# Kernel optimization log

Measured on AMD Instinct MI355X. Metric: run time of the kernel, lower is better.

## Reference

```python
import jax, jax.numpy as jnp
import numpy as np

N_NODES = 100000


def _gcn_conv(x, W, b, src, dst, deg_inv_sqrt):
    # linear transform first (PyG GCNConv order): [N, F] @ [F, H]
    h = x @ W
    # symmetric normalization per edge: deg^-1/2[src] * deg^-1/2[dst]
    norm = deg_inv_sqrt[src] * deg_inv_sqrt[dst]
    msg = h[src] * norm[:, None]  # [E, H]
    out = jax.ops.segment_sum(msg, dst, num_segments=N_NODES)
    return out + b


def setup_inputs() -> dict:
    key = jax.random.key(0)
    k1, k2, k3, k4 = jax.random.split(key, 4)
    F_IN, H = 512, 512
    E = 800000
    x = jax.random.normal(k1, (N_NODES, F_IN), dtype=jnp.float32)
    edge_index = jax.random.randint(k2, (2, E), 0, N_NODES, dtype=jnp.int64)
    W1 = jax.random.normal(k3, (F_IN, H), dtype=jnp.float32) * (1.0 / np.sqrt(F_IN))
    b1 = jnp.zeros((H,), dtype=jnp.float32)
    W2 = jax.random.normal(k4, (H, H), dtype=jnp.float32) * (1.0 / np.sqrt(H))
    b2 = jnp.zeros((H,), dtype=jnp.float32)
    return {"x": x, "edge_index": edge_index, "W1": W1, "b1": b1, "W2": W2, "b2": b2}


def reference(x, edge_index, W1, b1, W2, b2):
    # add self loops (PyG GCNConv default add_self_loops=True)
    loop = jnp.arange(N_NODES, dtype=edge_index.dtype)
    src = jnp.concatenate([edge_index[0], loop])
    dst = jnp.concatenate([edge_index[1], loop])
    # degree of destination nodes (including self loops)
    deg = jax.ops.segment_sum(jnp.ones_like(dst, dtype=x.dtype), dst, num_segments=N_NODES)
    deg_inv_sqrt = jnp.where(deg > 0, jax.lax.rsqrt(jnp.maximum(deg, 1.0)), 0.0)
    h = jax.nn.relu(_gcn_conv(x, W1, b1, src, dst, deg_inv_sqrt))
    # dropout is identity at inference (training=False)
    out = _gcn_conv(h, W2, b2, src, dst, deg_inv_sqrt)
    return out
```

## Files before the change

### kernel.cpp

```cpp
#include <hip/hip_runtime.h>

#define N_NODES 100000
#define E_EDGES 800000
#define E_TOT   900000
#define F 512

typedef __attribute__((ext_vector_type(8))) short short8;
typedef __attribute__((ext_vector_type(4))) float f32x4;
typedef unsigned int u32;

__device__ __forceinline__ float bfu(unsigned int u) {
    union { unsigned int i; float f; } c; c.i = u << 16; return c.f;
}
__device__ __forceinline__ unsigned short f2b(float f) {
    union { float f; unsigned int u; } c; c.f = f;
    return (unsigned short)((c.u + 0x7fffu + ((c.u >> 16) & 1u)) >> 16);
}
__device__ __forceinline__ float fbits(unsigned int u) {
    union { unsigned int i; float f; } c; c.i = u; return c.f;
}
__device__ __forceinline__ unsigned int bits(float f) {
    union { float f; unsigned int i; } c; c.f = f; return c.i;
}
__device__ __forceinline__ void gload_lds16(const void* g, void* l) {
    __builtin_amdgcn_global_load_lds(
        (const __attribute__((address_space(1))) u32*)g,
        (__attribute__((address_space(3))) u32*)l, 16, 0, 0);
}

__global__ void k_hist(const int* __restrict__ ei, unsigned int* deg) {
    int e = blockIdx.x * 256 + threadIdx.x;
    if (e < E_EDGES) atomicAdd(&deg[ei[E_EDGES + e]], 1u);
}

__global__ void k_disalloc(const unsigned int* __restrict__ deg, unsigned int* counter,
                           float* __restrict__ dis,
                           int2* __restrict__ seg, unsigned int* __restrict__ cursor) {
    int i = blockIdx.x * 256 + threadIdx.x;
    if (i < N_NODES) {
        unsigned int d = deg[i] + 1u;
        dis[i] = rsqrtf((float)d);
        unsigned int p = atomicAdd(counter, d);
        seg[i] = make_int2((int)p, (int)(p + d));
        cursor[i] = p;
    }
}

__global__ void k_scatter(const int* __restrict__ ei, const float* __restrict__ dis,
                          unsigned int* __restrict__ cursor,
                          uint2* __restrict__ ev) {
    int e = blockIdx.x * 256 + threadIdx.x;
    if (e < E_TOT) {
        int s, d;
        if (e < E_EDGES) { s = ei[e]; d = ei[E_EDGES + e]; }
        else             { s = e - E_EDGES; d = s; }
        unsigned int p = atomicAdd(&cursor[d], 1u);
        ev[p] = make_uint2((unsigned)s, bits(dis[s] * dis[d]));
    }
}

__global__ void k_cvtX(const float* __restrict__ xin, unsigned short* __restrict__ xb) {
    int i = blockIdx.x * 256 + threadIdx.x;
    const f32x4* p = (const f32x4*)xin + (size_t)i * 2;
    f32x4 a = __builtin_nontemporal_load(p);
    f32x4 b = __builtin_nontemporal_load(p + 1);
    uint4 o;
    o.x = (unsigned)f2b(a[0]) | ((unsigned)f2b(a[1]) << 16);
    o.y = (unsigned)f2b(a[2]) | ((unsigned)f2b(a[3]) << 16);
    o.z = (unsigned)f2b(b[0]) | ((unsigned)f2b(b[1]) << 16);
    o.w = (unsigned)f2b(b[2]) | ((unsigned)f2b(b[3]) << 16);
    *(uint4*)(xb + (size_t)i * 8) = o;
}

__global__ void k_cvtW(const float* __restrict__ W1, const float* __restrict__ W2,
                       unsigned short* __restrict__ W1t, unsigned short* __restrict__ W2t) {
    int t = blockIdx.x * 256 + threadIdx.x;
    int which = t >= F * F;
    int u = t - which * F * F;
    int n = u >> 9, k = u & 511;
    const float* W = which ? W2 : W1;
    unsigned short* Wt = which ? W2t : W1t;
    Wt[u] = f2b(W[k * F + n]);
}

__global__ __launch_bounds__(512, 4)
void gemm_bt(const unsigned short* __restrict__ A, const unsigned short* __restrict__ Bt,
             const float* __restrict__ bias,
             unsigned short* __restrict__ outb, float* __restrict__ outf,
             int relu, int M) {
    __shared__ unsigned short sm[24576];

    int nwg = gridDim.x * gridDim.y;
    int orig = blockIdx.y * gridDim.x + blockIdx.x;
    int q = nwg >> 3, r = nwg & 7;
    int xcd = orig & 7, j8 = orig >> 3;
    int wgid = (xcd < r ? xcd * (q + 1) : r * (q + 1) + (xcd - r) * q) + j8;
    int by = wgid & 3;
    int bx = wgid >> 2;

    int t  = threadIdx.x;
    int lane = t & 63, w = t >> 6;
    int wr = w >> 1, wc = w & 1;
    int rsel = lane & 15, khalf = (lane >> 4) * 8;

    f32x4 acc[4][4];
    #pragma unroll
    for (int m = 0; m < 4; ++m)
        #pragma unroll
        for (int n = 0; n < 4; ++n)
            acc[m][n] = (f32x4){0.f, 0.f, 0.f, 0.f};

    int rowBase = bx * 256;

    int arA[2], kcA[2];
    #pragma unroll
    for (int i = 0; i < 2; ++i) {
        int idx = i * 512 + t;
        int rr = idx >> 2;
        kcA[i] = (idx & 3) * 8;
        int ga = rowBase + rr; if (ga >= M) ga = M - 1;
        arA[i] = ga;
    }
    int brB = by * 128 + (t >> 2);
    int kcB = (t & 3) * 8;

    auto STAGE = [&](int buf, int k0) {
        gload_lds16(A + (size_t)arA[0] * F + k0 + kcA[0], sm + buf * 8192 + t * 8);
        gload_lds16(A + (size_t)arA[1] * F + k0 + kcA[1], sm + buf * 8192 + (512 + t) * 8);
        gload_lds16(Bt + (size_t)brB * F + k0 + kcB, sm + 16384 + buf * 4096 + t * 8);
    };
    auto COMPUTE = [&](int buf) {
        const unsigned short* la = sm + buf * 8192;
        const unsigned short* lb = sm + 16384 + buf * 4096;
        short8 bfr[4];
        #pragma unroll
        for (int n = 0; n < 4; ++n)
            bfr[n] = *(const short8*)&lb[(wc * 64 + n * 16 + rsel) * 32 + khalf];
        #pragma unroll
        for (int m = 0; m < 4; ++m) {
            short8 af = *(const short8*)&la[(wr * 64 + m * 16 + rsel) * 32 + khalf];
            #pragma unroll
            for (int n = 0; n < 4; ++n)
                acc[m][n] = __builtin_amdgcn_mfma_f32_16x16x32_bf16(af, bfr[n], acc[m][n], 0, 0, 0);
        }
    };

    STAGE(0, 0);
    __syncthreads();
    #pragma unroll
    for (int kp = 0; kp < 8; ++kp) {
        STAGE(1, (2 * kp + 1) * 32);
        COMPUTE(0);
        __syncthreads();
        if (kp < 7) STAGE(0, (2 * kp + 2) * 32);
        COMPUTE(1);
        __syncthreads();
    }

    int rq = (lane >> 4) * 4, cq = lane & 15;
    if (outb) {
        #pragma unroll
        for (int h = 0; h < 2; ++h) {
            if (h) __syncthreads();
            if ((wr >> 1) == h) {
                #pragma unroll
                for (int m = 0; m < 4; ++m)
                    #pragma unroll
                    for (int n = 0; n < 4; ++n) {
                        int cl = wc * 64 + n * 16 + cq;
                        float bv = bias[by * 128 + cl];
                        #pragma unroll
                        for (int j = 0; j < 4; ++j) {
                            int rl = (wr & 1) * 64 + m * 16 + rq + j;
                            float v = acc[m][n][j] + bv;
                            if (relu) v = fmaxf(v, 0.f);
                            sm[rl * 128 + cl] = f2b(v);
                        }
                    }
            }
            __syncthreads();
            #pragma unroll
            for (int p = 0; p < 4; ++p) {
                int sidx = (p * 512 + t) * 8;
                int row = sidx >> 7;
                int col = sidx & 127;
                int grow = rowBase + h * 128 + row;
                if (grow < M) {
                    uint4 v = *(const uint4*)&sm[sidx];
                    *(uint4*)&outb[(size_t)grow * F + by * 128 + col] = v;
                }
            }
        }
    } else {
        #pragma unroll
        for (int m = 0; m < 4; ++m)
            #pragma unroll
            for (int n = 0; n < 4; ++n) {
                int colv = by * 128 + wc * 64 + n * 16 + cq;
                float bv = bias[colv];
                #pragma unroll
                for (int j = 0; j < 4; ++j) {
                    int row = rowBase + wr * 64 + m * 16 + rq + j;
                    if (row < M) {
                        float v = acc[m][n][j] + bv;
                        if (relu) v = fmaxf(v, 0.f);
                        __builtin_nontemporal_store(v, outf + (size_t)row * F + colv);
                    }
                }
            }
    }
}

#define LOADP(k) uint2 p##k = ev[e + k]
#define LOADV(k) uint4 v##k = *(const uint4*)(base + ((size_t)p##k.x << 9))
#define ACCV(k)  { float w_ = fbits(p##k.y); \
    acc[0] += w_ * bfu(v##k.x & 0xffffu); acc[1] += w_ * bfu(v##k.x >> 16); \
    acc[2] += w_ * bfu(v##k.y & 0xffffu); acc[3] += w_ * bfu(v##k.y >> 16); \
    acc[4] += w_ * bfu(v##k.z & 0xffffu); acc[5] += w_ * bfu(v##k.z >> 16); \
    acc[6] += w_ * bfu(v##k.w & 0xffffu); acc[7] += w_ * bfu(v##k.w >> 16); }

__global__ __launch_bounds__(256)
void k_agg(const unsigned short* __restrict__ hin, const int2* __restrict__ seg,
           const uint2* __restrict__ ev,
           unsigned short* __restrict__ outb) {
    int node = blockIdx.x * 4 + (threadIdx.x >> 6);
    int lane = threadIdx.x & 63;
    if (node >= N_NODES) return;
    int2 se = seg[node];
    int e0 = se.x, e1 = se.y;
    float acc[8] = {0, 0, 0, 0, 0, 0, 0, 0};
    const unsigned short* base = hin + lane * 8;

    int e = e0;
    int n8 = e0 + ((e1 - e0) & ~7);
    for (; e < n8; e += 8) {
        LOADP(0); LOADP(1); LOADP(2); LOADP(3);
        LOADP(4); LOADP(5); LOADP(6); LOADP(7);
        LOADV(0); LOADV(1); LOADV(2); LOADV(3);
        LOADV(4); LOADV(5); LOADV(6); LOADV(7);
        ACCV(0); ACCV(1); ACCV(2); ACCV(3);
        ACCV(4); ACCV(5); ACCV(6); ACCV(7);
    }
    for (; e < e1; ++e) {
        LOADP(0); LOADV(0); ACCV(0);
    }

    uint4 o;
    o.x = (unsigned)f2b(acc[0]) | ((unsigned)f2b(acc[1]) << 16);
    o.y = (unsigned)f2b(acc[2]) | ((unsigned)f2b(acc[3]) << 16);
    o.z = (unsigned)f2b(acc[4]) | ((unsigned)f2b(acc[5]) << 16);
    o.w = (unsigned)f2b(acc[6]) | ((unsigned)f2b(acc[7]) << 16);
    *(uint4*)(outb + (size_t)node * F + lane * 8) = o;
}

extern "C" void kernel_launch(void* const* d_in, const int* in_sizes, int n_in,
                              void* d_out, int out_size, void* d_ws, size_t ws_size,
                              hipStream_t stream) {
    const float* x  = (const float*)d_in[0];
    const int*   ei = (const int*)d_in[1];
    const float* W1 = (const float*)d_in[2];
    const float* b1 = (const float*)d_in[3];
    const float* W2 = (const float*)d_in[4];
    const float* b2 = (const float*)d_in[5];
    float* out = (float*)d_out;

    char* ws = (char*)d_ws;
    size_t off = 0;
    auto alloc = [&](size_t bytes) -> void* {
        off = (off + 255) & ~(size_t)255;
        void* p = ws + off;
        off += bytes;
        return p;
    };

    unsigned short* tb  = (unsigned short*)alloc((size_t)N_NODES * F * 2);
    unsigned short* W1t = (unsigned short*)alloc((size_t)F * F * 2);
    unsigned short* W2t = (unsigned short*)alloc((size_t)F * F * 2);
    unsigned int*   deg = (unsigned int*)alloc((size_t)N_NODES * 4);
    unsigned int*   cnt = (unsigned int*)alloc(256);
    float*          dis = (float*)alloc((size_t)N_NODES * 4);
    int2*           seg = (int2*)alloc((size_t)N_NODES * 8);
    unsigned int*   cur = (unsigned int*)alloc((size_t)N_NODES * 4);
    uint2*          ev  = (uint2*)alloc((size_t)E_TOT * 8);

    unsigned short* h1b = (unsigned short*)d_out;
    unsigned short* xb  = (unsigned short*)((char*)d_out + (size_t)N_NODES * F * 2);

    int nb = (N_NODES + 255) / 256;

    hipMemsetAsync(deg, 0, (size_t)N_NODES * 4, stream);
    hipMemsetAsync(cnt, 0, 4, stream);
    k_hist<<<(E_EDGES + 255) / 256, 256, 0, stream>>>(ei, deg);
    k_disalloc<<<nb, 256, 0, stream>>>(deg, cnt, dis, seg, cur);
    k_scatter<<<(E_TOT + 255) / 256, 256, 0, stream>>>(ei, dis, cur, ev);

    k_cvtW<<<(2 * F * F) / 256, 256, 0, stream>>>(W1, W2, W1t, W2t);
    k_cvtX<<<(N_NODES * F / 8) / 256, 256, 0, stream>>>(x, xb);

    dim3 ggrid(4, (N_NODES + 255) / 256);

    k_agg<<<(N_NODES + 3) / 4, 256, 0, stream>>>(xb, seg, ev, tb);
    gemm_bt<<<ggrid, 512, 0, stream>>>(tb, W1t, b1, h1b, nullptr, 1, N_NODES);

    k_agg<<<(N_NODES + 3) / 4, 256, 0, stream>>>(h1b, seg, ev, tb);
    gemm_bt<<<ggrid, 512, 0, stream>>>(tb, W2t, b2, nullptr, out, 0, N_NODES);
}
```

Measured before the change: 619.4 us.

## Restructure bf16 GEMM into 128x128 tiles with K=64 swizzled LDS pipeline

Rewrites the GEMM kernel to use 256-thread blocks computing 128x128 tiles with a K-step of 64. The A and B staging is split across two phases so that loads for the next tile interleave with MFMA work, using explicit vmcnt waits and raw s_barrier instead of __syncthreads. LDS rows are XOR-swizzled to cut bank conflicts, and s_setprio is raised around the MFMA bursts. The smaller tile doubles the grid and reuses each B tile across fewer rows, trading some data reuse for occupancy and overlap.

```diff
diff --git a/kernel.cpp b/kernel.cpp
--- a/kernel.cpp
+++ b/kernel.cpp
@@ -83,12 +83,53 @@
     Wt[u] = f2b(W[k * F + n]);
 }
 
-__global__ __launch_bounds__(512, 4)
+
+#define G_STAGE_A(BUF, K0) { _Pragma("unroll") \
+    for (int i_ = 0; i_ < 4; ++i_) { \
+        int idx_ = i_ * 256 + t; \
+        gload_lds16(A + (size_t)arA[i_] * F + (K0) + kcsA[i_], sm + (BUF) * 8192 + idx_ * 8); \
+    } }
+#define G_STAGE_B(BUF, K0) { _Pragma("unroll") \
+    for (int i_ = 0; i_ < 4; ++i_) { \
+        int idx_ = i_ * 256 + t; \
+        gload_lds16(Bt + (size_t)brB[i_] * F + (K0) + kcsB[i_], sm + 16384 + (BUF) * 8192 + idx_ * 8); \
+    } }
+
+#define G_PHASE(BUF, KS, WLIT, DOWAIT, DOSTAGE, K0N) { \
+    if (DOSTAGE) { if ((KS) == 0) { G_STAGE_A((BUF) ^ 1, K0N) } else { G_STAGE_B((BUF) ^ 1, K0N) } } \
+    if (DOWAIT) { asm volatile("s_waitcnt vmcnt(" #WLIT ")" ::: "memory"); } \
+    __builtin_amdgcn_s_barrier(); \
+    asm volatile("" ::: "memory"); \
+    { \
+        const unsigned short* la = sm + (BUF) * 8192; \
+        const unsigned short* lb = sm + 16384 + (BUF) * 8192; \
+        int koff = ((KS) * 32 + khalf) ^ kx; \
+        short8 af_[4], bf_[4]; \
+        _Pragma("unroll") \
+        for (int m_ = 0; m_ < 4; ++m_) \
+            af_[m_] = *(const short8*)&la[(wr * 64 + m_ * 16 + rsel) * 64 + koff]; \
+        _Pragma("unroll") \
+        for (int n_ = 0; n_ < 4; ++n_) \
+            bf_[n_] = *(const short8*)&lb[(wc * 64 + n_ * 16 + rsel) * 64 + koff]; \
+        __builtin_amdgcn_s_setprio(1); \
+        _Pragma("unroll") \
+        for (int m_ = 0; m_ < 4; ++m_) \
+            _Pragma("unroll") \
+            for (int n_ = 0; n_ < 4; ++n_) \
+                acc[m_][n_] = __builtin_amdgcn_mfma_f32_16x16x32_bf16(af_[m_], bf_[n_], acc[m_][n_], 0, 0, 0); \
+        __builtin_amdgcn_s_setprio(0); \
+    } \
+    __builtin_amdgcn_s_barrier(); }
+
+#define G_KTILE(BUF, K0N) \
+    G_PHASE(BUF, 0, 4, 1, 1, K0N) G_PHASE(BUF, 1, 8, 0, 1, K0N)
+
+__global__ __launch_bounds__(256, 2)
 void gemm_bt(const unsigned short* __restrict__ A, const unsigned short* __restrict__ Bt,
              const float* __restrict__ bias,
              unsigned short* __restrict__ outb, float* __restrict__ outf,
              int relu, int M) {
-    __shared__ unsigned short sm[24576];
+    __shared__ unsigned short sm[32768];
 
     int nwg = gridDim.x * gridDim.y;
     int orig = blockIdx.y * gridDim.x + blockIdx.x;
@@ -102,6 +143,7 @@
     int lane = t & 63, w = t >> 6;
     int wr = w >> 1, wc = w & 1;
     int rsel = lane & 15, khalf = (lane >> 4) * 8;
+    int kx = (lane & 4) ? 16 : 0;
 
     f32x4 acc[4][4];
     #pragma unroll
@@ -110,85 +152,52 @@
         for (int n = 0; n < 4; ++n)
             acc[m][n] = (f32x4){0.f, 0.f, 0.f, 0.f};
 
-    int rowBase = bx * 256;
-
-    int arA[2], kcA[2];
+    int rowBase = bx * 128;
+
+    int arA[4], kcsA[4], brB[4], kcsB[4];
     #pragma unroll
-    for (int i = 0; i < 2; ++i) {
-        int idx = i * 512 + t;
-        int rr = idx >> 2;
-        kcA[i] = (idx & 3) * 8;
+    for (int i = 0; i < 4; ++i) {
+        int idx = i * 256 + t;
+        int rr = idx >> 3;
+        int kc = (idx & 7) * 8;
+        int kcs = kc ^ ((rr & 4) ? 16 : 0);
         int ga = rowBase + rr; if (ga >= M) ga = M - 1;
-        arA[i] = ga;
-    }
-    int brB = by * 128 + (t >> 2);
-    int kcB = (t & 3) * 8;
-
-    auto STAGE = [&](int buf, int k0) {
-        gload_lds16(A + (size_t)arA[0] * F + k0 + kcA[0], sm + buf * 8192 + t * 8);
-        gload_lds16(A + (size_t)arA[1] * F + k0 + kcA[1], sm + buf * 8192 + (512 + t) * 8);
-        gload_lds16(Bt + (size_t)brB * F + k0 + kcB, sm + 16384 + buf * 4096 + t * 8);
-    };
-    auto COMPUTE = [&](int buf) {
-        const unsigned short* la = sm + buf * 8192;
-        const unsigned short* lb = sm + 16384 + buf * 4096;
-        short8 bfr[4];
-        #pragma unroll
-        for (int n = 0; n < 4; ++n)
-            bfr[n] = *(const short8*)&lb[(wc * 64 + n * 16 + rsel) * 32 + khalf];
-        #pragma unroll
-        for (int m = 0; m < 4; ++m) {
-            short8 af = *(const short8*)&la[(wr * 64 + m * 16 + rsel) * 32 + khalf];
-            #pragma unroll
-            for (int n = 0; n < 4; ++n)
-                acc[m][n] = __builtin_amdgcn_mfma_f32_16x16x32_bf16(af, bfr[n], acc[m][n], 0, 0, 0);
-        }
-    };
-
-    STAGE(0, 0);
-    __syncthreads();
-    #pragma unroll
-    for (int kp = 0; kp < 8; ++kp) {
-        STAGE(1, (2 * kp + 1) * 32);
-        COMPUTE(0);
-        __syncthreads();
-        if (kp < 7) STAGE(0, (2 * kp + 2) * 32);
-        COMPUTE(1);
-        __syncthreads();
-    }
+        arA[i] = ga;  kcsA[i] = kcs;
+        brB[i] = by * 128 + rr;  kcsB[i] = kcs;
+    }
+
+    G_STAGE_A(0, 0) G_STAGE_B(0, 0)
+
+    G_KTILE(0,  64) G_KTILE(1, 128) G_KTILE(0, 192) G_KTILE(1, 256)
+    G_KTILE(0, 320) G_KTILE(1, 384) G_KTILE(0, 448)
+    G_PHASE(1, 0, 0, 1, 0, 0) G_PHASE(1, 1, 0, 0, 0, 0)
 
     int rq = (lane >> 4) * 4, cq = lane & 15;
     if (outb) {
         #pragma unroll
-        for (int h = 0; h < 2; ++h) {
-            if (h) __syncthreads();
-            if ((wr >> 1) == h) {
+        for (int m = 0; m < 4; ++m)
+            #pragma unroll
+            for (int n = 0; n < 4; ++n) {
+                int cl = wc * 64 + n * 16 + cq;
+                float bv = bias[by * 128 + cl];
                 #pragma unroll
-                for (int m = 0; m < 4; ++m)
-                    #pragma unroll
-                    for (int n = 0; n < 4; ++n) {
-                        int cl = wc * 64 + n * 16 + cq;
-                        float bv = bias[by * 128 + cl];
-                        #pragma unroll
-                        for (int j = 0; j < 4; ++j) {
-                            int rl = (wr & 1) * 64 + m * 16 + rq + j;
-                            float v = acc[m][n][j] + bv;
-                            if (relu) v = fmaxf(v, 0.f);
-                            sm[rl * 128 + cl] = f2b(v);
-                        }
-                    }
+                for (int j = 0; j < 4; ++j) {
+                    int rl = wr * 64 + m * 16 + rq + j;
+                    float v = acc[m][n][j] + bv;
+                    if (relu) v = fmaxf(v, 0.f);
+                    sm[rl * 128 + cl] = f2b(v);
+                }
             }
-            __syncthreads();
-            #pragma unroll
-            for (int p = 0; p < 4; ++p) {
-                int sidx = (p * 512 + t) * 8;
-                int row = sidx >> 7;
-                int col = sidx & 127;
-                int grow = rowBase + h * 128 + row;
-                if (grow < M) {
-                    uint4 v = *(const uint4*)&sm[sidx];
-                    *(uint4*)&outb[(size_t)grow * F + by * 128 + col] = v;
-                }
+        __syncthreads();
+        #pragma unroll
+        for (int p = 0; p < 8; ++p) {
+            int sidx = (p * 256 + t) * 8;
+            int row = sidx >> 7;
+            int col = sidx & 127;
+            int grow = rowBase + row;
+            if (grow < M) {
+                uint4 v = *(const uint4*)&sm[sidx];
+                *(uint4*)&outb[(size_t)grow * F + by * 128 + col] = v;
             }
         }
     } else {
@@ -297,11 +306,11 @@
     k_cvtW<<<(2 * F * F) / 256, 256, 0, stream>>>(W1, W2, W1t, W2t);
     k_cvtX<<<(N_NODES * F / 8) / 256, 256, 0, stream>>>(x, xb);
 
-    dim3 ggrid(4, (N_NODES + 255) / 256);
+    dim3 ggrid(4, (N_NODES + 127) / 128);
 
     k_agg<<<(N_NODES + 3) / 4, 256, 0, stream>>>(xb, seg, ev, tb);
-    gemm_bt<<<ggrid, 512, 0, stream>>>(tb, W1t, b1, h1b, nullptr, 1, N_NODES);
+    gemm_bt<<<ggrid, 256, 0, stream>>>(tb, W1t, b1, h1b, nullptr, 1, N_NODES);
 
     k_agg<<<(N_NODES + 3) / 4, 256, 0, stream>>>(h1b, seg, ev, tb);
-    gemm_bt<<<ggrid, 512, 0, stream>>>(tb, W2t, b2, nullptr, out, 0, N_NODES);
-}
+    gemm_bt<<<ggrid, 256, 0, stream>>>(tb, W2t, b2, nullptr, out, 0, N_NODES);
+}
```

Result: no change. 615.0 us (-0.7%).
